# Kernel optimization log

Measured on AMD Instinct MI355X. Metric: run time of the kernel, lower is better.

Reference implementation:

```python
import jax, jax.numpy as jnp
import numpy as np

B = 4096
N_FEAT = 4
VOCAB = 100000
EMB = 64
N_NEG = 3
TEMP = 1.0
EPS = 1e-8  # torch.cosine_similarity eps


def setup_inputs() -> dict:
    key = jax.random.key(0)
    ks = jax.random.split(key, 12)
    inp = {}
    inp['user_ids'] = jax.random.randint(ks[0], (B, N_FEAT), 0, VOCAB)
    inp['item_ids'] = jax.random.randint(ks[1], (B, N_FEAT), 0, VOCAB)
    inp['sw_ids'] = jax.random.randint(ks[2], (B,), 0, VOCAB)
    inp['user_tables'] = jax.random.normal(ks[3], (N_FEAT, VOCAB, EMB), jnp.float32) * 0.05
    inp['item_tables'] = jax.random.normal(ks[4], (N_FEAT, VOCAB, EMB), jnp.float32) * 0.05
    # sample weights must be positive (log is taken)
    inp['sw_table'] = jax.random.uniform(ks[5], (VOCAB,), jnp.float32) * 0.99 + 0.01
    inp['uW1'] = jax.random.normal(ks[6], (256, 256), jnp.float32) * 0.05
    inp['ub1'] = jnp.zeros((256,), jnp.float32)
    inp['uW2'] = jax.random.normal(ks[7], (256, 128), jnp.float32) * 0.05
    inp['ub2'] = jnp.zeros((128,), jnp.float32)
    inp['iW1'] = jax.random.normal(ks[8], (256, 256), jnp.float32) * 0.05
    inp['ib1'] = jnp.zeros((256,), jnp.float32)
    inp['iW2'] = jax.random.normal(ks[9], (256, 128), jnp.float32) * 0.05
    inp['ib2'] = jnp.zeros((128,), jnp.float32)
    return inp


def _embed(tables, ids):
    # tables: [F, V, E], ids: [B, F] -> [B, F*E]
    e = jax.vmap(lambda tbl, idx: tbl[idx], in_axes=(0, 1))(tables, ids)  # [F, B, E]
    return jnp.transpose(e, (1, 0, 2)).reshape(ids.shape[0], -1)


def _mlp(x, W1, b1, W2, b2):
    # torch-rechub MLP with output_layer=False: activation after every layer
    h = jax.nn.relu(x @ W1 + b1)
    return jax.nn.relu(h @ W2 + b2)


def reference(user_ids, item_ids, sw_ids, user_tables, item_tables, sw_table,
              uW1, ub1, uW2, ub2, iW1, ib1, iW2, ib2):
    u = _mlp(_embed(user_tables, user_ids), uW1, ub1, uW2, ub2)   # [B, 128]
    v = _mlp(_embed(item_tables, item_ids), iW1, ib1, iW2, ib2)   # [B, 128]
    un = u / jnp.maximum(jnp.linalg.norm(u, axis=-1, keepdims=True), EPS)
    vn = v / jnp.maximum(jnp.linalg.norm(v, axis=-1, keepdims=True), EPS)
    pred = un @ vn.T                                              # [B, B] cosine sim
    sw = sw_table[sw_ids]                                         # [B]
    scores = pred - jnp.log(sw)[None, :]                          # debias per item column
    # in-batch negative sampling: row i pairs with cols (i..i+n_neg) mod B
    rows = jnp.repeat(jnp.arange(B), N_NEG + 1)
    cols = ((jnp.arange(B)[:, None] + jnp.arange(N_NEG + 1)[None, :]) % B).reshape(-1)
    out = scores[rows, cols] / TEMP
    return out.reshape(B, N_NEG + 1)
```

## Files before the change

### kernel.cpp

```cpp
#include <hip/hip_runtime.h>
#include <math.h>

#define BATCH 4096
#define NFEAT 4
#define VOCAB 100000
#define EMB 64
#define D_IN 256
#define D_H 256
#define D_O 128
#define ROWS 16
#define XS_STRIDE 264
#define YS_STRIDE 132

typedef __attribute__((ext_vector_type(8))) short bf16x8;
typedef __attribute__((ext_vector_type(4))) float f32x4;

__device__ inline ushort f2bf(float f) {
  union { float f; unsigned u; } v; v.f = f;
  unsigned u = v.u;
  return (ushort)((u + 0x7fffu + ((u >> 16) & 1u)) >> 16);
}

__global__ __launch_bounds__(256) void prep_kernel(
    const float* __restrict__ uW1, const float* __restrict__ uW2,
    const float* __restrict__ iW1, const float* __restrict__ iW2,
    ushort* __restrict__ W1tu, ushort* __restrict__ W2tu,
    ushort* __restrict__ W1ti, ushort* __restrict__ W2ti) {
  int idx = blockIdx.x * 256 + threadIdx.x;
  if (idx < 65536) {
    int n = idx >> 8, k = idx & 255;
    W1tu[idx] = f2bf(uW1[k * 256 + n]);
  } else if (idx < 131072) {
    int j = idx - 65536; int n = j >> 8, k = j & 255;
    W1ti[j] = f2bf(iW1[k * 256 + n]);
  } else if (idx < 163840) {
    int j = idx - 131072; int n = j >> 8, k = j & 255;
    W2tu[j] = f2bf(uW2[k * 128 + n]);
  } else {
    int j = idx - 163840; int n = j >> 8, k = j & 255;
    W2ti[j] = f2bf(iW2[k * 128 + n]);
  }
}

__global__ __launch_bounds__(256) void tower_kernel(
    const int* __restrict__ user_ids, const int* __restrict__ item_ids,
    const float* __restrict__ user_tables, const float* __restrict__ item_tables,
    const ushort* __restrict__ W1tu, const float* __restrict__ ub1,
    const ushort* __restrict__ W2tu, const float* __restrict__ ub2,
    const ushort* __restrict__ W1ti, const float* __restrict__ ib1,
    const ushort* __restrict__ W2ti, const float* __restrict__ ib2,
    float* __restrict__ U, float* __restrict__ V) {
  const int tower = blockIdx.y;
  const int* ids = tower ? item_ids : user_ids;
  const float* tab = tower ? item_tables : user_tables;
  const ushort* W1t = tower ? W1ti : W1tu;
  const float* b1 = tower ? ib1 : ub1;
  const ushort* W2t = tower ? W2ti : W2tu;
  const float* b2 = tower ? ib2 : ub2;
  float* O = tower ? V : U;

  const int r0 = blockIdx.x * ROWS;
  const int tid = threadIdx.x;

  __shared__ ushort Xs[ROWS][XS_STRIDE];
  __shared__ ushort Hs[ROWS][XS_STRIDE];
  __shared__ float Ys[ROWS][YS_STRIDE];

#pragma unroll
  for (int i = 0; i < 4; i++) {
    int slot = i * 256 + tid;
    int row = slot >> 6;
    int c4 = slot & 63;
    int f = c4 >> 4;
    int id = ids[(size_t)(r0 + row) * NFEAT + f];
    float4 v = ((const float4*)(tab + ((size_t)f * VOCAB + (size_t)id) * EMB))[c4 & 15];
    ushort4 o = {f2bf(v.x), f2bf(v.y), f2bf(v.z), f2bf(v.w)};
    *(ushort4*)&Xs[row][c4 * 4] = o;
  }
  __syncthreads();

  const int lane = tid & 63;
  const int w = tid >> 6;
  const int m = lane & 15;
  const int quad = lane >> 4;

  {
    bf16x8 a[8];
#pragma unroll
    for (int k0 = 0; k0 < 8; k0++)
      a[k0] = *(const bf16x8*)&Xs[m][k0 * 32 + quad * 8];
#pragma unroll
    for (int ct = 0; ct < 4; ct++) {
      int n = (w * 4 + ct) * 16 + m;
      const ushort* wp = W1t + (size_t)n * 256 + quad * 8;
      f32x4 acc = {0.f, 0.f, 0.f, 0.f};
#pragma unroll
      for (int k0 = 0; k0 < 8; k0++)
        acc = __builtin_amdgcn_mfma_f32_16x16x32_bf16(
            a[k0], *(const bf16x8*)(wp + k0 * 32), acc, 0, 0, 0);
      float bias = b1[n];
#pragma unroll
      for (int reg = 0; reg < 4; reg++) {
        int r = quad * 4 + reg;
        Hs[r][n] = f2bf(fmaxf(acc[reg] + bias, 0.f));
      }
    }
  }
  __syncthreads();

  {
    bf16x8 h[8];
#pragma unroll
    for (int k0 = 0; k0 < 8; k0++)
      h[k0] = *(const bf16x8*)&Hs[m][k0 * 32 + quad * 8];
#pragma unroll
    for (int ct = 0; ct < 2; ct++) {
      int n = (w * 2 + ct) * 16 + m;
      const ushort* wp = W2t + (size_t)n * 256 + quad * 8;
      f32x4 acc = {0.f, 0.f, 0.f, 0.f};
#pragma unroll
      for (int k0 = 0; k0 < 8; k0++)
        acc = __builtin_amdgcn_mfma_f32_16x16x32_bf16(
            h[k0], *(const bf16x8*)(wp + k0 * 32), acc, 0, 0, 0);
      float bias = b2[n];
#pragma unroll
      for (int reg = 0; reg < 4; reg++) {
        int r = quad * 4 + reg;
        Ys[r][n] = fmaxf(acc[reg] + bias, 0.f);
      }
    }
  }
  __syncthreads();

#pragma unroll
  for (int rr = 0; rr < 4; rr++) {
    int row = w * 4 + rr;
    float y0 = Ys[row][lane];
    float y1 = Ys[row][64 + lane];
    float s = y0 * y0 + y1 * y1;
#pragma unroll
    for (int off = 32; off; off >>= 1) s += __shfl_xor(s, off);
    float inv = 1.f / fmaxf(sqrtf(s), 1e-8f);
    float* op = O + (size_t)(r0 + row) * D_O;
    op[lane] = y0 * inv;
    op[64 + lane] = y1 * inv;
  }
}

__global__ __launch_bounds__(256) void score_kernel(
    const float* __restrict__ U, const float* __restrict__ V,
    const int* __restrict__ sw_ids, const float* __restrict__ sw_table,
    float* __restrict__ out) {
  int wave = threadIdx.x >> 6;
  int lane = threadIdx.x & 63;
  int i = blockIdx.x * 4 + wave;

  float u0 = U[(size_t)i * D_O + lane];
  float u1 = U[(size_t)i * D_O + 64 + lane];

#pragma unroll
  for (int j = 0; j < 4; j++) {
    int c = (i + j) & (BATCH - 1);
    float v0 = V[(size_t)c * D_O + lane];
    float v1 = V[(size_t)c * D_O + 64 + lane];
    float d = u0 * v0 + u1 * v1;
#pragma unroll
    for (int off = 32; off; off >>= 1) d += __shfl_xor(d, off);
    if (lane == 0) {
      out[(size_t)i * 4 + j] = d - logf(sw_table[sw_ids[c]]);
    }
  }
}

extern "C" void kernel_launch(void* const* d_in, const int* in_sizes, int n_in,
                              void* d_out, int out_size, void* d_ws, size_t ws_size,
                              hipStream_t stream) {
  (void)in_sizes; (void)n_in; (void)out_size; (void)ws_size;
  const int*   user_ids    = (const int*)d_in[0];
  const int*   item_ids    = (const int*)d_in[1];
  const int*   sw_ids      = (const int*)d_in[2];
  const float* user_tables = (const float*)d_in[3];
  const float* item_tables = (const float*)d_in[4];
  const float* sw_table    = (const float*)d_in[5];
  const float* uW1 = (const float*)d_in[6];
  const float* ub1 = (const float*)d_in[7];
  const float* uW2 = (const float*)d_in[8];
  const float* ub2 = (const float*)d_in[9];
  const float* iW1 = (const float*)d_in[10];
  const float* ib1 = (const float*)d_in[11];
  const float* iW2 = (const float*)d_in[12];
  const float* ib2 = (const float*)d_in[13];
  float* out = (float*)d_out;

  float* U = (float*)d_ws;
  float* V = U + (size_t)BATCH * D_O;
  ushort* W1tu = (ushort*)(V + (size_t)BATCH * D_O);
  ushort* W1ti = W1tu + 256 * 256;
  ushort* W2tu = W1ti + 256 * 256;
  ushort* W2ti = W2tu + 128 * 256;

  prep_kernel<<<768, 256, 0, stream>>>(uW1, uW2, iW1, iW2, W1tu, W2tu, W1ti, W2ti);

  tower_kernel<<<dim3(BATCH / ROWS, 2), 256, 0, stream>>>(
      user_ids, item_ids, user_tables, item_tables,
      W1tu, ub1, W2tu, ub2, W1ti, ib1, W2ti, ib2, U, V);

  score_kernel<<<BATCH / 4, 256, 0, stream>>>(U, V, sw_ids, sw_table, out);
}
```

Baseline: 216.1 us.

## Fuse prep, tower and score kernels into one cooperative kernel with grid syncs

Replaces the three separate launches (weight transpose/convert, two-tower MLP, scoring) with a single cooperative kernel of 512 blocks that uses grid-wide syncs between phases. The aim is to remove the launch overhead and inter-kernel gaps of three small kernels. In exchange it adds two grid barriers, and the prep phase now runs on fewer blocks with a strided loop. The cooperative launch also requires all 512 blocks to be co-resident.

```diff
diff --git a/kernel.cpp b/kernel.cpp
--- a/kernel.cpp
+++ b/kernel.cpp
@@ -1,5 +1,8 @@
 #include <hip/hip_runtime.h>
+#include <hip/hip_cooperative_groups.h>
 #include <math.h>
+
+namespace cg = cooperative_groups;
 
 #define BATCH 4096
 #define NFEAT 4
@@ -11,6 +14,7 @@
 #define ROWS 16
 #define XS_STRIDE 264
 #define YS_STRIDE 132
+#define GRID_BLKS 512
 
 typedef __attribute__((ext_vector_type(8))) short bf16x8;
 typedef __attribute__((ext_vector_type(4))) float f32x4;
@@ -21,153 +25,156 @@
   return (ushort)((u + 0x7fffu + ((u >> 16) & 1u)) >> 16);
 }
 
-__global__ __launch_bounds__(256) void prep_kernel(
-    const float* __restrict__ uW1, const float* __restrict__ uW2,
-    const float* __restrict__ iW1, const float* __restrict__ iW2,
+__global__ __launch_bounds__(256) void fused_kernel(
+    const int* __restrict__ user_ids, const int* __restrict__ item_ids,
+    const int* __restrict__ sw_ids,
+    const float* __restrict__ user_tables, const float* __restrict__ item_tables,
+    const float* __restrict__ sw_table,
+    const float* __restrict__ uW1, const float* __restrict__ ub1,
+    const float* __restrict__ uW2, const float* __restrict__ ub2,
+    const float* __restrict__ iW1, const float* __restrict__ ib1,
+    const float* __restrict__ iW2, const float* __restrict__ ib2,
     ushort* __restrict__ W1tu, ushort* __restrict__ W2tu,
-    ushort* __restrict__ W1ti, ushort* __restrict__ W2ti) {
-  int idx = blockIdx.x * 256 + threadIdx.x;
-  if (idx < 65536) {
-    int n = idx >> 8, k = idx & 255;
-    W1tu[idx] = f2bf(uW1[k * 256 + n]);
-  } else if (idx < 131072) {
-    int j = idx - 65536; int n = j >> 8, k = j & 255;
-    W1ti[j] = f2bf(iW1[k * 256 + n]);
-  } else if (idx < 163840) {
-    int j = idx - 131072; int n = j >> 8, k = j & 255;
-    W2tu[j] = f2bf(uW2[k * 128 + n]);
-  } else {
-    int j = idx - 163840; int n = j >> 8, k = j & 255;
-    W2ti[j] = f2bf(iW2[k * 128 + n]);
+    ushort* __restrict__ W1ti, ushort* __restrict__ W2ti,
+    float* __restrict__ U, float* __restrict__ V, float* __restrict__ out) {
+  cg::grid_group grid = cg::this_grid();
+  const int tid = threadIdx.x;
+
+  for (int idx = blockIdx.x * 256 + tid; idx < 196608; idx += GRID_BLKS * 256) {
+    if (idx < 65536) {
+      int n = idx >> 8, k = idx & 255;
+      W1tu[idx] = f2bf(uW1[k * 256 + n]);
+    } else if (idx < 131072) {
+      int j = idx - 65536; int n = j >> 8, k = j & 255;
+      W1ti[j] = f2bf(iW1[k * 256 + n]);
+    } else if (idx < 163840) {
+      int j = idx - 131072; int n = j >> 8, k = j & 255;
+      W2tu[j] = f2bf(uW2[k * 128 + n]);
+    } else {
+      int j = idx - 163840; int n = j >> 8, k = j & 255;
+      W2ti[j] = f2bf(iW2[k * 128 + n]);
+    }
   }
-}
-
-__global__ __launch_bounds__(256) void tower_kernel(
-    const int* __restrict__ user_ids, const int* __restrict__ item_ids,
-    const float* __restrict__ user_tables, const float* __restrict__ item_tables,
-    const ushort* __restrict__ W1tu, const float* __restrict__ ub1,
-    const ushort* __restrict__ W2tu, const float* __restrict__ ub2,
-    const ushort* __restrict__ W1ti, const float* __restrict__ ib1,
-    const ushort* __restrict__ W2ti, const float* __restrict__ ib2,
-    float* __restrict__ U, float* __restrict__ V) {
-  const int tower = blockIdx.y;
-  const int* ids = tower ? item_ids : user_ids;
-  const float* tab = tower ? item_tables : user_tables;
-  const ushort* W1t = tower ? W1ti : W1tu;
-  const float* b1 = tower ? ib1 : ub1;
-  const ushort* W2t = tower ? W2ti : W2tu;
-  const float* b2 = tower ? ib2 : ub2;
-  float* O = tower ? V : U;
-
-  const int r0 = blockIdx.x * ROWS;
-  const int tid = threadIdx.x;
+  grid.sync();
 
   __shared__ ushort Xs[ROWS][XS_STRIDE];
   __shared__ ushort Hs[ROWS][XS_STRIDE];
   __shared__ float Ys[ROWS][YS_STRIDE];
-
-#pragma unroll
-  for (int i = 0; i < 4; i++) {
-    int slot = i * 256 + tid;
-    int row = slot >> 6;
-    int c4 = slot & 63;
-    int f = c4 >> 4;
-    int id = ids[(size_t)(r0 + row) * NFEAT + f];
-    float4 v = ((const float4*)(tab + ((size_t)f * VOCAB + (size_t)id) * EMB))[c4 & 15];
-    ushort4 o = {f2bf(v.x), f2bf(v.y), f2bf(v.z), f2bf(v.w)};
-    *(ushort4*)&Xs[row][c4 * 4] = o;
+  {
+    const int tower = blockIdx.x >> 8;
+    const int tile = blockIdx.x & 255;
+    const int* ids = tower ? item_ids : user_ids;
+    const float* tab = tower ? item_tables : user_tables;
+    const ushort* W1t = tower ? W1ti : W1tu;
+    const float* b1 = tower ? ib1 : ub1;
+    const ushort* W2t = tower ? W2ti : W2tu;
+    const float* b2 = tower ? ib2 : ub2;
+    float* O = tower ? V : U;
+    const int r0 = tile * ROWS;
+
+#pragma unroll
+    for (int i = 0; i < 4; i++) {
+      int slot = i * 256 + tid;
+      int row = slot >> 6;
+      int c4 = slot & 63;
+      int f = c4 >> 4;
+      int id = ids[(size_t)(r0 + row) * NFEAT + f];
+      float4 v = ((const float4*)(tab + ((size_t)f * VOCAB + (size_t)id) * EMB))[c4 & 15];
+      ushort4 o = {f2bf(v.x), f2bf(v.y), f2bf(v.z), f2bf(v.w)};
+      *(ushort4*)&Xs[row][c4 * 4] = o;
+    }
+    __syncthreads();
+
+    const int lane = tid & 63;
+    const int w = tid >> 6;
+    const int m = lane & 15;
+    const int quad = lane >> 4;
+
+    {
+      bf16x8 a[8];
+#pragma unroll
+      for (int k0 = 0; k0 < 8; k0++)
+        a[k0] = *(const bf16x8*)&Xs[m][k0 * 32 + quad * 8];
+#pragma unroll
+      for (int ct = 0; ct < 4; ct++) {
+        int n = (w * 4 + ct) * 16 + m;
+        const ushort* wp = W1t + (size_t)n * 256 + quad * 8;
+        f32x4 acc = {0.f, 0.f, 0.f, 0.f};
+#pragma unroll
+        for (int k0 = 0; k0 < 8; k0++)
+          acc = __builtin_amdgcn_mfma_f32_16x16x32_bf16(
+              a[k0], *(const bf16x8*)(wp + k0 * 32), acc, 0, 0, 0);
+        float bias = b1[n];
+#pragma unroll
+        for (int reg = 0; reg < 4; reg++) {
+          int r = quad * 4 + reg;
+          Hs[r][n] = f2bf(fmaxf(acc[reg] + bias, 0.f));
+        }
+      }
+    }
+    __syncthreads();
+
+    {
+      bf16x8 h[8];
+#pragma unroll
+      for (int k0 = 0; k0 < 8; k0++)
+        h[k0] = *(const bf16x8*)&Hs[m][k0 * 32 + quad * 8];
+#pragma unroll
+      for (int ct = 0; ct < 2; ct++) {
+        int n = (w * 2 + ct) * 16 + m;
+        const ushort* wp = W2t + (size_t)n * 256 + quad * 8;
+        f32x4 acc = {0.f, 0.f, 0.f, 0.f};
+#pragma unroll
+        for (int k0 = 0; k0 < 8; k0++)
+          acc = __builtin_amdgcn_mfma_f32_16x16x32_bf16(
+              h[k0], *(const bf16x8*)(wp + k0 * 32), acc, 0, 0, 0);
+        float bias = b2[n];
+#pragma unroll
+        for (int reg = 0; reg < 4; reg++) {
+          int r = quad * 4 + reg;
+          Ys[r][n] = fmaxf(acc[reg] + bias, 0.f);
+        }
+      }
+    }
+    __syncthreads();
+
+#pragma unroll
+    for (int rr = 0; rr < 4; rr++) {
+      int row = w * 4 + rr;
+      float y0 = Ys[row][lane];
+      float y1 = Ys[row][64 + lane];
+      float s = y0 * y0 + y1 * y1;
+#pragma unroll
+      for (int off = 32; off; off >>= 1) s += __shfl_xor(s, off);
+      float inv = 1.f / fmaxf(sqrtf(s), 1e-8f);
+      float* op = O + (size_t)(r0 + row) * D_O;
+      op[lane] = y0 * inv;
+      op[64 + lane] = y1 * inv;
+    }
   }
-  __syncthreads();
-
-  const int lane = tid & 63;
-  const int w = tid >> 6;
-  const int m = lane & 15;
-  const int quad = lane >> 4;
+  grid.sync();
 
   {
-    bf16x8 a[8];
-#pragma unroll
-    for (int k0 = 0; k0 < 8; k0++)
-      a[k0] = *(const bf16x8*)&Xs[m][k0 * 32 + quad * 8];
-#pragma unroll
-    for (int ct = 0; ct < 4; ct++) {
-      int n = (w * 4 + ct) * 16 + m;
-      const ushort* wp = W1t + (size_t)n * 256 + quad * 8;
-      f32x4 acc = {0.f, 0.f, 0.f, 0.f};
-#pragma unroll
-      for (int k0 = 0; k0 < 8; k0++)
-        acc = __builtin_amdgcn_mfma_f32_16x16x32_bf16(
-            a[k0], *(const bf16x8*)(wp + k0 * 32), acc, 0, 0, 0);
-      float bias = b1[n];
-#pragma unroll
-      for (int reg = 0; reg < 4; reg++) {
-        int r = quad * 4 + reg;
-        Hs[r][n] = f2bf(fmaxf(acc[reg] + bias, 0.f));
+    const int lane = tid & 63;
+    const int w = tid >> 6;
+    const int wave_id = blockIdx.x * 4 + w;
+#pragma unroll
+    for (int rr = 0; rr < 2; rr++) {
+      int i = wave_id * 2 + rr;
+      float u0 = U[(size_t)i * D_O + lane];
+      float u1 = U[(size_t)i * D_O + 64 + lane];
+#pragma unroll
+      for (int j = 0; j < 4; j++) {
+        int c = (i + j) & (BATCH - 1);
+        float v0 = V[(size_t)c * D_O + lane];
+        float v1 = V[(size_t)c * D_O + 64 + lane];
+        float d = u0 * v0 + u1 * v1;
+#pragma unroll
+        for (int off = 32; off; off >>= 1) d += __shfl_xor(d, off);
+        if (lane == 0) {
+          out[(size_t)i * 4 + j] = d - logf(sw_table[sw_ids[c]]);
+        }
       }
-    }
-  }
-  __syncthreads();
-
-  {
-    bf16x8 h[8];
-#pragma unroll
-    for (int k0 = 0; k0 < 8; k0++)
-      h[k0] = *(const bf16x8*)&Hs[m][k0 * 32 + quad * 8];
-#pragma unroll
-    for (int ct = 0; ct < 2; ct++) {
-      int n = (w * 2 + ct) * 16 + m;
-      const ushort* wp = W2t + (size_t)n * 256 + quad * 8;
-      f32x4 acc = {0.f, 0.f, 0.f, 0.f};
-#pragma unroll
-      for (int k0 = 0; k0 < 8; k0++)
-        acc = __builtin_amdgcn_mfma_f32_16x16x32_bf16(
-            h[k0], *(const bf16x8*)(wp + k0 * 32), acc, 0, 0, 0);
-      float bias = b2[n];
-#pragma unroll
-      for (int reg = 0; reg < 4; reg++) {
-        int r = quad * 4 + reg;
-        Ys[r][n] = fmaxf(acc[reg] + bias, 0.f);
-      }
-    }
-  }
-  __syncthreads();
-
-#pragma unroll
-  for (int rr = 0; rr < 4; rr++) {
-    int row = w * 4 + rr;
-    float y0 = Ys[row][lane];
-    float y1 = Ys[row][64 + lane];
-    float s = y0 * y0 + y1 * y1;
-#pragma unroll
-    for (int off = 32; off; off >>= 1) s += __shfl_xor(s, off);
-    float inv = 1.f / fmaxf(sqrtf(s), 1e-8f);
-    float* op = O + (size_t)(r0 + row) * D_O;
-    op[lane] = y0 * inv;
-    op[64 + lane] = y1 * inv;
-  }
-}
-
-__global__ __launch_bounds__(256) void score_kernel(
-    const float* __restrict__ U, const float* __restrict__ V,
-    const int* __restrict__ sw_ids, const float* __restrict__ sw_table,
-    float* __restrict__ out) {
-  int wave = threadIdx.x >> 6;
-  int lane = threadIdx.x & 63;
-  int i = blockIdx.x * 4 + wave;
-
-  float u0 = U[(size_t)i * D_O + lane];
-  float u1 = U[(size_t)i * D_O + 64 + lane];
-
-#pragma unroll
-  for (int j = 0; j < 4; j++) {
-    int c = (i + j) & (BATCH - 1);
-    float v0 = V[(size_t)c * D_O + lane];
-    float v1 = V[(size_t)c * D_O + 64 + lane];
-    float d = u0 * v0 + u1 * v1;
-#pragma unroll
-    for (int off = 32; off; off >>= 1) d += __shfl_xor(d, off);
-    if (lane == 0) {
-      out[(size_t)i * 4 + j] = d - logf(sw_table[sw_ids[c]]);
     }
   }
 }
@@ -199,11 +206,13 @@
   ushort* W2tu = W1ti + 256 * 256;
   ushort* W2ti = W2tu + 128 * 256;
 
-  prep_kernel<<<768, 256, 0, stream>>>(uW1, uW2, iW1, iW2, W1tu, W2tu, W1ti, W2ti);
-
-  tower_kernel<<<dim3(BATCH / ROWS, 2), 256, 0, stream>>>(
-      user_ids, item_ids, user_tables, item_tables,
-      W1tu, ub1, W2tu, ub2, W1ti, ib1, W2ti, ib2, U, V);
-
-  score_kernel<<<BATCH / 4, 256, 0, stream>>>(U, V, sw_ids, sw_table, out);
+  void* args[] = {
+      (void*)&user_ids, (void*)&item_ids, (void*)&sw_ids,
+      (void*)&user_tables, (void*)&item_tables, (void*)&sw_table,
+      (void*)&uW1, (void*)&ub1, (void*)&uW2, (void*)&ub2,
+      (void*)&iW1, (void*)&ib1, (void*)&iW2, (void*)&ib2,
+      (void*)&W1tu, (void*)&W2tu, (void*)&W1ti, (void*)&W2ti,
+      (void*)&U, (void*)&V, (void*)&out};
+  hipLaunchCooperativeKernel((const void*)fused_kernel, dim3(GRID_BLKS),
+                             dim3(256), args, 0, stream);
 }
```

Result: slower. 344.2 us (+59.3%).
